# Kernel optimization log

Measured on AMD Instinct MI355X. Metric: run time of the kernel, lower is better.

## Reference

```python
import jax, jax.numpy as jnp
import numpy as np

N = 8192
D_IN, D_H, D_OUT = 512, 256, 128
BETA = 0.8
EPS = 1e-08


def _xavier(key, fan_in, fan_out):
    limit = float(np.sqrt(6.0 / (fan_in + fan_out)))
    return jax.random.uniform(key, (fan_in, fan_out), jnp.float32, -limit, limit)


def setup_inputs() -> dict:
    key = jax.random.key(0)
    kA, kS, kx, kw1, kw2 = jax.random.split(key, 5)
    A = jax.random.uniform(kA, (N, N), jnp.float32)
    S = jax.random.uniform(kS, (N, N), jnp.float32)
    x = jax.random.normal(kx, (N, D_IN), jnp.float32)
    W1 = _xavier(kw1, D_IN, D_H)
    b1 = jnp.zeros((D_H,), jnp.float32)
    W2 = _xavier(kw2, D_H, D_OUT)
    b2 = jnp.zeros((D_OUT,), jnp.float32)
    return {"A": A, "S": S, "x": x, "W1": W1, "b1": b1, "W2": W2, "b2": b2}


def _normalize_adj(adj):
    # adj + eps * I  (add only on the diagonal; no dense eye materialized)
    idx = jnp.arange(adj.shape[0])
    adj = adj.at[idx, idx].add(EPS)
    d = adj.sum(axis=1)                       # [N]
    d_inv_sqrt = d ** -0.5
    d_inv_sqrt = jnp.where(jnp.isinf(d_inv_sqrt), 0.0, d_inv_sqrt)
    # D^{-1/2} A D^{-1/2} as broadcast row/col scaling (same math as diag matmuls)
    return d_inv_sqrt[:, None] * adj * d_inv_sqrt[None, :]


def reference(A, S, x, W1, b1, W2, b2):
    A_tilde = A + BETA * S                    # [N, N]
    A_norm = _normalize_adj(A_tilde)          # [N, N]
    # GCN layer 1: relu(A_norm @ (x @ W1) + b1)   (dropout is identity at eval)
    h = jax.nn.relu(A_norm @ (x @ W1) + b1)   # [N, D_H]
    # GCN layer 2 (output layer, no activation)
    out = A_norm @ (h @ W2) + b2              # [N, D_OUT]
    return out
```

## Files before the change

### kernel.cpp

```cpp
#include <hip/hip_runtime.h>

#define EPS 1e-8f
#define BETA 0.8f

typedef __attribute__((ext_vector_type(8))) short bf16x8;
typedef __attribute__((ext_vector_type(4))) float f32x4;
typedef __attribute__((ext_vector_type(4))) float float4v;
typedef __attribute__((ext_vector_type(4))) unsigned short ushort4v;

__device__ __forceinline__ unsigned short f2b(float f) {
  unsigned int u = __builtin_bit_cast(unsigned int, f);
  u += 0x7fffu + ((u >> 16) & 1u);
  return (unsigned short)(u >> 16);
}

__global__ __launch_bounds__(256) void k_degree_convert(
    const float* __restrict__ A, const float* __restrict__ S,
    unsigned short* __restrict__ At, float* __restrict__ dis) {
  const int row = blockIdx.x;
  const int tid = threadIdx.x;
  const size_t base = (size_t)row * 8192;
  float4v a[8], s[8];
#pragma unroll
  for (int i = 0; i < 8; ++i) {
    const int c = i * 1024 + tid * 4;
    a[i] = __builtin_nontemporal_load(
        reinterpret_cast<const float4v*>(A + base + c));
    s[i] = __builtin_nontemporal_load(
        reinterpret_cast<const float4v*>(S + base + c));
  }
  float sum = 0.f;
#pragma unroll
  for (int i = 0; i < 8; ++i) {
    const int c = i * 1024 + tid * 4;
    float v0 = a[i].x + BETA * s[i].x;
    float v1 = a[i].y + BETA * s[i].y;
    float v2 = a[i].z + BETA * s[i].z;
    float v3 = a[i].w + BETA * s[i].w;
    sum += (v0 + v1) + (v2 + v3);
    ushort4v o = {f2b(v0), f2b(v1), f2b(v2), f2b(v3)};
    *reinterpret_cast<ushort4v*>(At + base + c) = o;
  }
#pragma unroll
  for (int off = 32; off > 0; off >>= 1) sum += __shfl_xor(sum, off, 64);
  __shared__ float wsum[4];
  if ((tid & 63) == 0) wsum[tid >> 6] = sum;
  __syncthreads();
  if (tid == 0) {
    float d = ((wsum[0] + wsum[1]) + (wsum[2] + wsum[3])) + EPS;
    dis[row] = (d > 0.f) ? 1.0f / sqrtf(d) : 0.f;
  }
}

__global__ __launch_bounds__(256) void k_conv_all(
    const float* __restrict__ x, unsigned short* __restrict__ xb,
    const float* __restrict__ W1, unsigned short* __restrict__ W1T,
    const float* __restrict__ W2, unsigned short* __restrict__ W2T) {
  const int b = blockIdx.x;
  if (b < 4096) {
    const int idx = b * 256 + threadIdx.x;
    float4v v = reinterpret_cast<const float4v*>(x)[idx];
    ushort4v o = {f2b(v.x), f2b(v.y), f2b(v.z), f2b(v.w)};
    reinterpret_cast<ushort4v*>(xb)[idx] = o;
  } else if (b < 4608) {
    const int idx = (b - 4096) * 256 + threadIdx.x;
    const int r = idx >> 8, c = idx & 255;
    W1T[c * 512 + r] = f2b(W1[idx]);
  } else {
    const int idx = (b - 4608) * 256 + threadIdx.x;
    const int r = idx >> 7, c = idx & 127;
    W2T[c * 256 + r] = f2b(W2[idx]);
  }
}

template <int BM, int BN, int EPI>
__global__ __launch_bounds__(256) void k_gemm_bt(
    const unsigned short* __restrict__ Ag, const unsigned short* __restrict__ BTg,
    int M, int N, int Kstride, int Kchunk,
    const float* __restrict__ dis, const float* __restrict__ bias,
    float* __restrict__ outf, unsigned short* __restrict__ outb) {
  constexpr int WM = BM / 2, WN = BN / 2;
  constexpr int MF = WM / 16, NF = WN / 16;
  constexpr int NLOADS = BM / 32 + BN / 32;
  __shared__ unsigned short Als[2][BM][64];
  __shared__ unsigned short Bls[2][BN][64];
  const int tid = threadIdx.x;
  const int lane = tid & 63;
  const int wm = (tid >> 6) >> 1, wn = (tid >> 6) & 1;
  const int brow = blockIdx.x * BM, bcol = blockIdx.y * BN;
  const int ar = tid >> 3;
  const int ac = (tid & 7) * 8;
  const int l15 = lane & 15, lk = (lane >> 4) * 8;

  f32x4 acc[MF][NF];
#pragma unroll
  for (int i = 0; i < MF; ++i)
#pragma unroll
    for (int j = 0; j < NF; ++j) acc[i][j] = (f32x4){0.f, 0.f, 0.f, 0.f};

  auto stage = [&](int buf, int k0) {
#pragma unroll
    for (int i = 0; i < BM / 32; ++i) {
      const unsigned short* g =
          Ag + (size_t)(brow + i * 32 + ar) * Kstride + k0 + ac;
      __builtin_amdgcn_global_load_lds(
          (const __attribute__((address_space(1))) void*)g,
          (__attribute__((address_space(3))) void*)&Als[buf][i * 32 + ar][ac],
          16, 0, 0);
    }
#pragma unroll
    for (int i = 0; i < BN / 32; ++i) {
      const unsigned short* g =
          BTg + (size_t)(bcol + i * 32 + ar) * Kstride + k0 + ac;
      __builtin_amdgcn_global_load_lds(
          (const __attribute__((address_space(1))) void*)g,
          (__attribute__((address_space(3))) void*)&Bls[buf][i * 32 + ar][ac],
          16, 0, 0);
    }
  };

  const int nsteps = Kchunk / 64;
  stage(0, 0);
  for (int t = 0; t < nsteps; ++t) {
    const int cur = t & 1;
    if (t + 1 < nsteps) {
      stage(cur ^ 1, (t + 1) * 64);
      asm volatile("s_waitcnt vmcnt(%0)" ::"n"(NLOADS));
    } else {
      asm volatile("s_waitcnt vmcnt(0)");
    }
    __builtin_amdgcn_s_barrier();
    asm volatile("" ::: "memory");
#pragma unroll
    for (int kk = 0; kk < 2; ++kk) {
      bf16x8 afr[MF], bfr[NF];
#pragma unroll
      for (int mi = 0; mi < MF; ++mi)
        afr[mi] = *reinterpret_cast<const bf16x8*>(
            &Als[cur][wm * WM + mi * 16 + l15][kk * 32 + lk]);
#pragma unroll
      for (int ni = 0; ni < NF; ++ni)
        bfr[ni] = *reinterpret_cast<const bf16x8*>(
            &Bls[cur][wn * WN + ni * 16 + l15][kk * 32 + lk]);
#pragma unroll
      for (int mi = 0; mi < MF; ++mi)
#pragma unroll
        for (int ni = 0; ni < NF; ++ni)
          acc[mi][ni] = __builtin_amdgcn_mfma_f32_16x16x32_bf16(
              afr[mi], bfr[ni], acc[mi][ni], 0, 0, 0);
    }
    asm volatile("" ::: "memory");
    __builtin_amdgcn_s_barrier();
  }

  const int crow0 = brow + wm * WM, ccol0 = bcol + wn * WN;
#pragma unroll
  for (int mi = 0; mi < MF; ++mi) {
    const int row0 = crow0 + mi * 16 + (lane >> 4) * 4;
    const float d0 = dis[row0], d1 = dis[row0 + 1], d2 = dis[row0 + 2],
                d3 = dis[row0 + 3];
#pragma unroll
    for (int ni = 0; ni < NF; ++ni) {
      const int col = ccol0 + ni * 16 + l15;
      f32x4 a = acc[mi][ni];
      if constexpr (EPI == 0) {
        ushort4v o = {f2b(d0 * a.x), f2b(d1 * a.y), f2b(d2 * a.z),
                      f2b(d3 * a.w)};
        *reinterpret_cast<ushort4v*>(outb + (size_t)col * M + row0) = o;
      } else if constexpr (EPI == 1) {
        const float bb = bias[col];
        float v0 = d0 * a.x + bb; v0 = v0 > 0.f ? v0 : 0.f;
        float v1 = d1 * a.y + bb; v1 = v1 > 0.f ? v1 : 0.f;
        float v2 = d2 * a.z + bb; v2 = v2 > 0.f ? v2 : 0.f;
        float v3 = d3 * a.w + bb; v3 = v3 > 0.f ? v3 : 0.f;
        outb[(size_t)(row0 + 0) * N + col] = f2b(v0);
        outb[(size_t)(row0 + 1) * N + col] = f2b(v1);
        outb[(size_t)(row0 + 2) * N + col] = f2b(v2);
        outb[(size_t)(row0 + 3) * N + col] = f2b(v3);
      } else {
        const float bb = bias[col];
        outf[(size_t)(row0 + 0) * N + col] = d0 * a.x + bb;
        outf[(size_t)(row0 + 1) * N + col] = d1 * a.y + bb;
        outf[(size_t)(row0 + 2) * N + col] = d2 * a.z + bb;
        outf[(size_t)(row0 + 3) * N + col] = d3 * a.w + bb;
      }
    }
  }
}

template <int BM, int BN, int WGM, int WGN>
__global__ __launch_bounds__(512, 2) void k_gemm_split(
    const unsigned short* __restrict__ Ag,
    const unsigned short* __restrict__ BTg,
    int M, int N, int Kstride, int Kchunk, int gx,
    float* __restrict__ P) {
  constexpr int NLOADS = BM / 64 + BN / 64;
  __shared__ unsigned short Als[3][BM][64];
  __shared__ unsigned short Bls[3][BN][64];

  const int nblk = gridDim.x;
  const int flat = blockIdx.x;
  const int cpx = nblk >> 3;
  const int swz = (flat & 7) * cpx + (flat >> 3);
  const int bx = swz % gx;
  const int bz = swz / gx;

  const int tid = threadIdx.x;
  const int lane = tid & 63;
  const int wid = tid >> 6;
  const int wm = wid / WGN, wn = wid % WGN;
  const int brow = bx * BM;
  const int kbase = bz * Kchunk;
  const int ar = tid >> 3;
  const int acs = ((tid & 7) ^ (ar & 7)) * 8;
  const int l15 = lane & 15;
  const int lk = (lane >> 4) * 8;
  const int rk = (l15 & 7) * 8;

  f32x4 acc[4][4];
#pragma unroll
  for (int i = 0; i < 4; ++i)
#pragma unroll
    for (int j = 0; j < 4; ++j) acc[i][j] = (f32x4){0.f, 0.f, 0.f, 0.f};

  auto stage = [&](int buf, int k0) {
#pragma unroll
    for (int i = 0; i < BM / 64; ++i) {
      const unsigned short* g =
          Ag + (size_t)(brow + i * 64 + ar) * Kstride + k0 + acs;
      __builtin_amdgcn_global_load_lds(
          (const __attribute__((address_space(1))) void*)g,
          (__attribute__((address_space(3))) void*)
              &Als[buf][i * 64 + ar][(tid & 7) * 8],
          16, 0, 0);
    }
#pragma unroll
    for (int i = 0; i < BN / 64; ++i) {
      const unsigned short* g =
          BTg + (size_t)(i * 64 + ar) * Kstride + k0 + acs;
      __builtin_amdgcn_global_load_lds(
          (const __attribute__((address_space(1))) void*)g,
          (__attribute__((address_space(3))) void*)
              &Bls[buf][i * 64 + ar][(tid & 7) * 8],
          16, 0, 0);
    }
  };

  const int nsteps = Kchunk / 64;
  stage(0, kbase);
  stage(1, kbase + 64);
  for (int t = 0; t < nsteps; ++t) {
    const int cur = t % 3;
    if (t + 2 < nsteps) {
      stage((t + 2) % 3, kbase + (t + 2) * 64);
      asm volatile("s_waitcnt vmcnt(%0)" ::"n"(2 * NLOADS));
    } else if (t + 1 < nsteps) {
      asm volatile("s_waitcnt vmcnt(%0)" ::"n"(NLOADS));
    } else {
      asm volatile("s_waitcnt vmcnt(0)");
    }
    __builtin_amdgcn_s_barrier();
    asm volatile("" ::: "memory");
#pragma unroll
    for (int kk = 0; kk < 2; ++kk) {
      bf16x8 afr[4], bfr[4];
#pragma unroll
      for (int mi = 0; mi < 4; ++mi)
        afr[mi] = *reinterpret_cast<const bf16x8*>(
            &Als[cur][wm * 64 + mi * 16 + l15][(kk * 32 + lk) ^ rk]);
#pragma unroll
      for (int ni = 0; ni < 4; ++ni)
        bfr[ni] = *reinterpret_cast<const bf16x8*>(
            &Bls[cur][wn * 64 + ni * 16 + l15][(kk * 32 + lk) ^ rk]);
      __builtin_amdgcn_s_setprio(1);
#pragma unroll
      for (int mi = 0; mi < 4; ++mi)
#pragma unroll
        for (int ni = 0; ni < 4; ++ni)
          acc[mi][ni] = __builtin_amdgcn_mfma_f32_16x16x32_bf16(
              afr[mi], bfr[ni], acc[mi][ni], 0, 0, 0);
      __builtin_amdgcn_s_setprio(0);
    }
    asm volatile("" ::: "memory");
    __builtin_amdgcn_s_barrier();
  }

  float* Pz = P + (size_t)bz * M * N;
  const int crow0 = brow + wm * 64, ccol0 = wn * 64;
#pragma unroll
  for (int mi = 0; mi < 4; ++mi) {
    const int row0 = crow0 + mi * 16 + (lane >> 4) * 4;
#pragma unroll
    for (int ni = 0; ni < 4; ++ni) {
      const int col = ccol0 + ni * 16 + l15;
      f32x4 a = acc[mi][ni];
      Pz[(size_t)(row0 + 0) * N + col] = a.x;
      Pz[(size_t)(row0 + 1) * N + col] = a.y;
      Pz[(size_t)(row0 + 2) * N + col] = a.z;
      Pz[(size_t)(row0 + 3) * N + col] = a.w;
    }
  }
}

template <int MODE, int NS>
__global__ __launch_bounds__(256) void k_reduceN(
    const float* __restrict__ P, int M, int N,
    const float* __restrict__ dis, const float* __restrict__ bias,
    unsigned short* __restrict__ outb, float* __restrict__ outf) {
  const int idx = blockIdx.x * 256 + threadIdx.x;
  const int row = idx / (N / 4);
  const int c0 = (idx - row * (N / 4)) * 4;
  const size_t off = (size_t)row * N + c0;
  const size_t ps = (size_t)M * N;
  float r0 = 0.f, r1 = 0.f, r2 = 0.f, r3 = 0.f;
#pragma unroll
  for (int z = 0; z < NS; ++z) {
    float4v v = *reinterpret_cast<const float4v*>(P + z * ps + off);
    r0 += v.x; r1 += v.y; r2 += v.z; r3 += v.w;
  }
  const float d = dis[row];
  float4v bb = *reinterpret_cast<const float4v*>(bias + c0);
  r0 = d * r0 + bb.x; r1 = d * r1 + bb.y;
  r2 = d * r2 + bb.z; r3 = d * r3 + bb.w;
  if constexpr (MODE == 0) {
    r0 = r0 > 0.f ? r0 : 0.f;
    r1 = r1 > 0.f ? r1 : 0.f;
    r2 = r2 > 0.f ? r2 : 0.f;
    r3 = r3 > 0.f ? r3 : 0.f;
    ushort4v o = {f2b(r0), f2b(r1), f2b(r2), f2b(r3)};
    *reinterpret_cast<ushort4v*>(outb + off) = o;
  } else {
    float4v o = {r0, r1, r2, r3};
    *reinterpret_cast<float4v*>(outf + off) = o;
  }
}

extern "C" void kernel_launch(void* const* d_in, const int* in_sizes, int n_in,
                              void* d_out, int out_size, void* d_ws,
                              size_t ws_size, hipStream_t stream) {
  const float* A  = (const float*)d_in[0];
  const float* S  = (const float*)d_in[1];
  const float* x  = (const float*)d_in[2];
  const float* W1 = (const float*)d_in[3];
  const float* b1 = (const float*)d_in[4];
  const float* W2 = (const float*)d_in[5];
  const float* b2 = (const float*)d_in[6];
  float* out = (float*)d_out;

  char* ws = (char*)d_ws;
  dim3 blk(256);

  const size_t O_At = 0, O_xb = 134217728, O_M1T = 142606336,
               O_P = 146800640, O_W1T = 180355072, O_W2T = 180617216,
               O_dis = 180682752, NEED = 180715520;

  if (ws_size >= NEED) {
    unsigned short* At  = (unsigned short*)(ws + O_At);
    unsigned short* xb  = (unsigned short*)(ws + O_xb);
    unsigned short* M1T = (unsigned short*)(ws + O_M1T);
    float*          P   = (float*)(ws + O_P);
    unsigned short* hb  = (unsigned short*)(ws + O_M1T);
    unsigned short* M2T = (unsigned short*)(ws + O_xb);
    unsigned short* W1T = (unsigned short*)(ws + O_W1T);
    unsigned short* W2T = (unsigned short*)(ws + O_W2T);
    float*          dis = (float*)(ws + O_dis);

    k_degree_convert<<<8192, blk, 0, stream>>>(A, S, At, dis);
    k_conv_all<<<4736, blk, 0, stream>>>(x, xb, W1, W1T, W2, W2T);
    k_gemm_bt<128, 64, 0><<<dim3(64, 4), blk, 0, stream>>>(
        xb, W1T, 8192, 256, 512, 512, dis, nullptr, nullptr, M1T);
    k_gemm_split<128, 256, 2, 4><<<dim3(256), dim3(512), 0, stream>>>(
        At, M1T, 8192, 256, 8192, 2048, 64, P);
    k_reduceN<0, 4><<<2048, blk, 0, stream>>>(P, 8192, 256, dis, b1, hb,
                                              nullptr);
    k_gemm_bt<64, 64, 0><<<dim3(128, 2), blk, 0, stream>>>(
        hb, W2T, 8192, 128, 256, 256, dis, nullptr, nullptr, M2T);
    k_gemm_split<256, 128, 4, 2><<<dim3(256), dim3(512), 0, stream>>>(
        At, M2T, 8192, 128, 8192, 1024, 32, P);
    k_reduceN<1, 8><<<1024, blk, 0, stream>>>(P, 8192, 128, dis, b2, nullptr,
                                              out);
  } else {
    unsigned short* At  = (unsigned short*)(ws);
    unsigned short* xb  = (unsigned short*)(ws + 134217728);
    unsigned short* M1T = (unsigned short*)(ws + 142606336);
    unsigned short* hb  = (unsigned short*)(ws + 146800640);
    unsigned short* M2T = (unsigned short*)(ws + 150994944);
    unsigned short* W1T = (unsigned short*)(ws + 153092096);
    unsigned short* W2T = (unsigned short*)(ws + 153354240);
    float* dis          = (float*)(ws + 153419776);

    k_degree_convert<<<8192, blk, 0, stream>>>(A, S, At, dis);
    k_conv_all<<<4736, blk, 0, stream>>>(x, xb, W1, W1T, W2, W2T);
    k_gemm_bt<128, 64, 0><<<dim3(64, 4), blk, 0, stream>>>(
        xb, W1T, 8192, 256, 512, 512, dis, nullptr, nullptr, M1T);
    k_gemm_bt<128, 64, 1><<<dim3(64, 4), blk, 0, stream>>>(
        At, M1T, 8192, 256, 8192, 8192, dis, b1, nullptr, hb);
    k_gemm_bt<64, 64, 0><<<dim3(128, 2), blk, 0, stream>>>(
        hb, W2T, 8192, 128, 256, 256, dis, nullptr, nullptr, M2T);
    k_gemm_bt<64, 64, 2><<<dim3(128, 2), blk, 0, stream>>>(
        At, M2T, 8192, 128, 8192, 8192, dis, b2, out, nullptr);
  }
}
```

Before: 220.8 us.

## Fuse split-K reduce into h@W2 GEMM and merge conversion kernels

Adds a kernel that reduces the four split-K partials of layer 1, applies degree scaling, bias and ReLU, and keeps h in LDS as bf16. It then multiplies h by W2 with MFMA and writes the scaled transposed M2T directly. This removes the materialised hb buffer and one kernel launch. The degree/convert kernel and the x/W conversion kernel are also merged into one launch. The cost is a large LDS footprint (W2 tile plus h tile) that may limit occupancy.

```diff
diff --git a/kernel.cpp b/kernel.cpp
--- a/kernel.cpp
+++ b/kernel.cpp
@@ -14,41 +14,62 @@
   return (unsigned short)(u >> 16);
 }
 
-__global__ __launch_bounds__(256) void k_degree_convert(
+__global__ __launch_bounds__(256) void k_degree_conv(
     const float* __restrict__ A, const float* __restrict__ S,
-    unsigned short* __restrict__ At, float* __restrict__ dis) {
-  const int row = blockIdx.x;
+    unsigned short* __restrict__ At, float* __restrict__ dis,
+    const float* __restrict__ x, unsigned short* __restrict__ xb,
+    const float* __restrict__ W1, unsigned short* __restrict__ W1T,
+    const float* __restrict__ W2, unsigned short* __restrict__ W2T) {
+  __shared__ float wsum[4];
   const int tid = threadIdx.x;
-  const size_t base = (size_t)row * 8192;
-  float4v a[8], s[8];
-#pragma unroll
-  for (int i = 0; i < 8; ++i) {
-    const int c = i * 1024 + tid * 4;
-    a[i] = __builtin_nontemporal_load(
-        reinterpret_cast<const float4v*>(A + base + c));
-    s[i] = __builtin_nontemporal_load(
-        reinterpret_cast<const float4v*>(S + base + c));
-  }
-  float sum = 0.f;
-#pragma unroll
-  for (int i = 0; i < 8; ++i) {
-    const int c = i * 1024 + tid * 4;
-    float v0 = a[i].x + BETA * s[i].x;
-    float v1 = a[i].y + BETA * s[i].y;
-    float v2 = a[i].z + BETA * s[i].z;
-    float v3 = a[i].w + BETA * s[i].w;
-    sum += (v0 + v1) + (v2 + v3);
-    ushort4v o = {f2b(v0), f2b(v1), f2b(v2), f2b(v3)};
-    *reinterpret_cast<ushort4v*>(At + base + c) = o;
-  }
-#pragma unroll
-  for (int off = 32; off > 0; off >>= 1) sum += __shfl_xor(sum, off, 64);
-  __shared__ float wsum[4];
-  if ((tid & 63) == 0) wsum[tid >> 6] = sum;
-  __syncthreads();
-  if (tid == 0) {
-    float d = ((wsum[0] + wsum[1]) + (wsum[2] + wsum[3])) + EPS;
-    dis[row] = (d > 0.f) ? 1.0f / sqrtf(d) : 0.f;
+  if (blockIdx.x < 8192) {
+    const int row = blockIdx.x;
+    const size_t base = (size_t)row * 8192;
+    float4v a[8], s[8];
+#pragma unroll
+    for (int i = 0; i < 8; ++i) {
+      const int c = i * 1024 + tid * 4;
+      a[i] = __builtin_nontemporal_load(
+          reinterpret_cast<const float4v*>(A + base + c));
+      s[i] = __builtin_nontemporal_load(
+          reinterpret_cast<const float4v*>(S + base + c));
+    }
+    float sum = 0.f;
+#pragma unroll
+    for (int i = 0; i < 8; ++i) {
+      const int c = i * 1024 + tid * 4;
+      float v0 = a[i].x + BETA * s[i].x;
+      float v1 = a[i].y + BETA * s[i].y;
+      float v2 = a[i].z + BETA * s[i].z;
+      float v3 = a[i].w + BETA * s[i].w;
+      sum += (v0 + v1) + (v2 + v3);
+      ushort4v o = {f2b(v0), f2b(v1), f2b(v2), f2b(v3)};
+      *reinterpret_cast<ushort4v*>(At + base + c) = o;
+    }
+#pragma unroll
+    for (int off = 32; off > 0; off >>= 1) sum += __shfl_xor(sum, off, 64);
+    if ((tid & 63) == 0) wsum[tid >> 6] = sum;
+    __syncthreads();
+    if (tid == 0) {
+      float d = ((wsum[0] + wsum[1]) + (wsum[2] + wsum[3])) + EPS;
+      dis[row] = (d > 0.f) ? 1.0f / sqrtf(d) : 0.f;
+    }
+  } else {
+    const int b = blockIdx.x - 8192;
+    if (b < 4096) {
+      const int idx = b * 256 + tid;
+      float4v v = reinterpret_cast<const float4v*>(x)[idx];
+      ushort4v o = {f2b(v.x), f2b(v.y), f2b(v.z), f2b(v.w)};
+      reinterpret_cast<ushort4v*>(xb)[idx] = o;
+    } else if (b < 4608) {
+      const int idx = (b - 4096) * 256 + tid;
+      const int r = idx >> 8, c = idx & 255;
+      W1T[c * 512 + r] = f2b(W1[idx]);
+    } else {
+      const int idx = (b - 4608) * 256 + tid;
+      const int r = idx >> 7, c = idx & 127;
+      W2T[c * 256 + r] = f2b(W2[idx]);
+    }
   }
 }
 
@@ -70,6 +91,44 @@
     const int idx = (b - 4608) * 256 + threadIdx.x;
     const int r = idx >> 7, c = idx & 127;
     W2T[c * 256 + r] = f2b(W2[idx]);
+  }
+}
+
+__global__ __launch_bounds__(256) void k_degree_convert(
+    const float* __restrict__ A, const float* __restrict__ S,
+    unsigned short* __restrict__ At, float* __restrict__ dis) {
+  const int row = blockIdx.x;
+  const int tid = threadIdx.x;
+  const size_t base = (size_t)row * 8192;
+  float4v a[8], s[8];
+#pragma unroll
+  for (int i = 0; i < 8; ++i) {
+    const int c = i * 1024 + tid * 4;
+    a[i] = __builtin_nontemporal_load(
+        reinterpret_cast<const float4v*>(A + base + c));
+    s[i] = __builtin_nontemporal_load(
+        reinterpret_cast<const float4v*>(S + base + c));
+  }
+  float sum = 0.f;
+#pragma unroll
+  for (int i = 0; i < 8; ++i) {
+    const int c = i * 1024 + tid * 4;
+    float v0 = a[i].x + BETA * s[i].x;
+    float v1 = a[i].y + BETA * s[i].y;
+    float v2 = a[i].z + BETA * s[i].z;
+    float v3 = a[i].w + BETA * s[i].w;
+    sum += (v0 + v1) + (v2 + v3);
+    ushort4v o = {f2b(v0), f2b(v1), f2b(v2), f2b(v3)};
+    *reinterpret_cast<ushort4v*>(At + base + c) = o;
+  }
+#pragma unroll
+  for (int off = 32; off > 0; off >>= 1) sum += __shfl_xor(sum, off, 64);
+  __shared__ float wsum[4];
+  if ((tid & 63) == 0) wsum[tid >> 6] = sum;
+  __syncthreads();
+  if (tid == 0) {
+    float d = ((wsum[0] + wsum[1]) + (wsum[2] + wsum[3])) + EPS;
+    dis[row] = (d > 0.f) ? 1.0f / sqrtf(d) : 0.f;
   }
 }
 
@@ -302,6 +361,111 @@
   }
 }
 
+__global__ __launch_bounds__(256, 2) void k_h_gemm(
+    const float* __restrict__ P,
+    const unsigned short* __restrict__ W2T,
+    const float* __restrict__ dis, const float* __restrict__ b1,
+    unsigned short* __restrict__ M2T) {
+  __shared__ unsigned short W2ls[128][256];
+  __shared__ unsigned short hls[32][256];
+  const int tid = threadIdx.x;
+  const int lane = tid & 63;
+  const int l15 = lane & 15;
+  const int wid = tid >> 6;
+  const int m0 = blockIdx.x * 32;
+
+  {
+    const int wr = tid >> 5, wc = tid & 31;
+#pragma unroll
+    for (int i = 0; i < 16; ++i) {
+      const int row = i * 8 + wr;
+      const unsigned short* g = W2T + row * 256 + ((wc ^ (row & 7)) * 8);
+      __builtin_amdgcn_global_load_lds(
+          (const __attribute__((address_space(1))) void*)g,
+          (__attribute__((address_space(3))) void*)&W2ls[row][wc * 8], 16, 0,
+          0);
+    }
+  }
+
+  {
+    const int col4 = (lane | (wid << 6)) & 255;
+  }
+  {
+    const int col4 = (tid & 63) * 4;
+    const int rsub = tid >> 6;
+    const float4v bv = *reinterpret_cast<const float4v*>(b1 + col4);
+    const int ch = (tid & 63) >> 1;
+    const int sub = (tid & 1) * 4;
+#pragma unroll
+    for (int p = 0; p < 8; ++p) {
+      const int row = p * 4 + rsub;
+      const size_t off = (size_t)(m0 + row) * 256 + col4;
+      float4v v0 = *reinterpret_cast<const float4v*>(P + off);
+      float4v v1 = *reinterpret_cast<const float4v*>(P + 2097152 + off);
+      float4v v2 = *reinterpret_cast<const float4v*>(P + 4194304 + off);
+      float4v v3 = *reinterpret_cast<const float4v*>(P + 6291456 + off);
+      const float dm = dis[m0 + row];
+      float r0 = dm * ((v0.x + v1.x) + (v2.x + v3.x)) + bv.x;
+      float r1 = dm * ((v0.y + v1.y) + (v2.y + v3.y)) + bv.y;
+      float r2 = dm * ((v0.z + v1.z) + (v2.z + v3.z)) + bv.z;
+      float r3 = dm * ((v0.w + v1.w) + (v2.w + v3.w)) + bv.w;
+      r0 = r0 > 0.f ? r0 : 0.f;
+      r1 = r1 > 0.f ? r1 : 0.f;
+      r2 = r2 > 0.f ? r2 : 0.f;
+      r3 = r3 > 0.f ? r3 : 0.f;
+      ushort4v o = {f2b(r0), f2b(r1), f2b(r2), f2b(r3)};
+      *reinterpret_cast<ushort4v*>(
+          &hls[row][(ch ^ (row & 7)) * 8 + sub]) = o;
+    }
+  }
+  __syncthreads();
+
+  f32x4 acc[2][2];
+#pragma unroll
+  for (int i = 0; i < 2; ++i)
+#pragma unroll
+    for (int j = 0; j < 2; ++j) acc[i][j] = (f32x4){0.f, 0.f, 0.f, 0.f};
+
+#pragma unroll
+  for (int kk = 0; kk < 8; ++kk) {
+    const int gch = kk * 4 + (lane >> 4);
+    bf16x8 a[2], b[2];
+#pragma unroll
+    for (int mi = 0; mi < 2; ++mi) {
+      const int mr = mi * 16 + l15;
+      a[mi] =
+          *reinterpret_cast<const bf16x8*>(&hls[mr][(gch ^ (mr & 7)) * 8]);
+    }
+#pragma unroll
+    for (int ni = 0; ni < 2; ++ni) {
+      const int nr = wid * 32 + ni * 16 + l15;
+      b[ni] =
+          *reinterpret_cast<const bf16x8*>(&W2ls[nr][(gch ^ (nr & 7)) * 8]);
+    }
+#pragma unroll
+    for (int mi = 0; mi < 2; ++mi)
+#pragma unroll
+      for (int ni = 0; ni < 2; ++ni)
+        acc[mi][ni] = __builtin_amdgcn_mfma_f32_16x16x32_bf16(
+            a[mi], b[ni], acc[mi][ni], 0, 0, 0);
+  }
+
+#pragma unroll
+  for (int mi = 0; mi < 2; ++mi) {
+    const int r0 = mi * 16 + (lane >> 4) * 4;
+    const float d0 = dis[m0 + r0], d1 = dis[m0 + r0 + 1],
+                d2 = dis[m0 + r0 + 2], d3 = dis[m0 + r0 + 3];
+#pragma unroll
+    for (int ni = 0; ni < 2; ++ni) {
+      const int col = wid * 32 + ni * 16 + l15;
+      f32x4 a = acc[mi][ni];
+      ushort4v o = {f2b(d0 * a.x), f2b(d1 * a.y), f2b(d2 * a.z),
+                    f2b(d3 * a.w)};
+      *reinterpret_cast<ushort4v*>(&M2T[(size_t)col * 8192 + m0 + r0]) = o;
+    }
+  }
+}
+
 template <int MODE, int NS>
 __global__ __launch_bounds__(256) void k_reduceN(
     const float* __restrict__ P, int M, int N,
@@ -359,22 +523,18 @@
     unsigned short* xb  = (unsigned short*)(ws + O_xb);
     unsigned short* M1T = (unsigned short*)(ws + O_M1T);
     float*          P   = (float*)(ws + O_P);
-    unsigned short* hb  = (unsigned short*)(ws + O_M1T);
     unsigned short* M2T = (unsigned short*)(ws + O_xb);
     unsigned short* W1T = (unsigned short*)(ws + O_W1T);
     unsigned short* W2T = (unsigned short*)(ws + O_W2T);
     float*          dis = (float*)(ws + O_dis);
 
-    k_degree_convert<<<8192, blk, 0, stream>>>(A, S, At, dis);
-    k_conv_all<<<4736, blk, 0, stream>>>(x, xb, W1, W1T, W2, W2T);
+    k_degree_conv<<<12928, blk, 0, stream>>>(A, S, At, dis, x, xb, W1, W1T,
+                                             W2, W2T);
     k_gemm_bt<128, 64, 0><<<dim3(64, 4), blk, 0, stream>>>(
         xb, W1T, 8192, 256, 512, 512, dis, nullptr, nullptr, M1T);
     k_gemm_split<128, 256, 2, 4><<<dim3(256), dim3(512), 0, stream>>>(
         At, M1T, 8192, 256, 8192, 2048, 64, P);
-    k_reduceN<0, 4><<<2048, blk, 0, stream>>>(P, 8192, 256, dis, b1, hb,
-                                              nullptr);
-    k_gemm_bt<64, 64, 0><<<dim3(128, 2), blk, 0, stream>>>(
-        hb, W2T, 8192, 128, 256, 256, dis, nullptr, nullptr, M2T);
+    k_h_gemm<<<256, blk, 0, stream>>>(P, W2T, dis, b1, M2T);
     k_gemm_split<256, 128, 4, 2><<<dim3(256), dim3(512), 0, stream>>>(
         At, M2T, 8192, 128, 8192, 1024, 32, P);
     k_reduceN<1, 8><<<1024, blk, 0, stream>>>(P, 8192, 128, dis, b2, nullptr,
```

New measurement: 212.8 us. 3.6% less time.
